# Kernel optimization log

Hardware: AMD Instinct MI355X
Metric: run time of the kernel (lower is better)

Reference implementation:

```python
import jax, jax.numpy as jnp
import numpy as np

B, S, E, H = 2, 2048, 1024, 16
D = E // H  # head dim = 64


def setup_inputs() -> dict:
    key = jax.random.key(0)
    ks = jax.random.split(key, 8)
    return {
        "query": jax.random.normal(ks[0], (B, S, E), dtype=jnp.float32),
        "key": jax.random.normal(ks[1], (B, S, E), dtype=jnp.float32),
        "value": jax.random.normal(ks[2], (B, S, E), dtype=jnp.float32),
        "qkv_weight": jax.random.normal(ks[3], (3 * E, E), dtype=jnp.float32) * 0.02,
        "qkv_bias": jax.random.normal(ks[4], (3 * E,), dtype=jnp.float32) * 0.02,
        "proj_weight": jax.random.normal(ks[5], (E, E), dtype=jnp.float32) * 0.02,
        "proj_bias": jax.random.normal(ks[6], (E,), dtype=jnp.float32) * 0.02,
        "mask": jax.random.normal(ks[7], (S, S), dtype=jnp.float32),
    }


def reference(query, key, value, qkv_weight, qkv_bias, proj_weight, proj_bias, mask):
    # Split fused QKV weight/bias into per-projection chunks ([E,E] each).
    wq, wk, wv = jnp.split(qkv_weight, 3, axis=0)
    bq, bk, bv = jnp.split(qkv_bias, 3, axis=0)

    def proj_heads(x, w, b):
        # [B,S,E] @ [E,E]^T + [E] -> [B,H,S,D]
        y = jnp.einsum("bse,fe->bsf", x, w) + b
        return y.reshape(B, S, H, D).transpose(0, 2, 1, 3)

    q = proj_heads(query, wq, bq)
    k = proj_heads(key, wk, bk)
    v = proj_heads(value, wv, bv)

    scale = 1.0 / jnp.sqrt(jnp.asarray(D, dtype=q.dtype))
    # scores: [B,H,S,S]; mask_type 0 -> additive [S,S] float mask broadcast over B,H
    scores = jnp.einsum("bhsd,bhtd->bhst", q, k) * scale + mask[None, None, :, :]
    attn = jax.nn.softmax(scores, axis=-1)
    ctx = jnp.einsum("bhst,bhtd->bhsd", attn, v)  # [B,H,S,D]
    ctx = ctx.transpose(0, 2, 1, 3).reshape(B, S, E)
    # output projection
    return jnp.einsum("bse,fe->bsf", ctx, proj_weight) + proj_bias
```

## Files before the change

### kernel.cpp

```cpp
#include <hip/hip_runtime.h>
#include <hip/hip_bf16.h>

typedef unsigned short u16;
typedef __attribute__((ext_vector_type(8))) __bf16 bf16x8;
typedef __attribute__((ext_vector_type(4))) __bf16 bf16x4;
typedef __attribute__((ext_vector_type(4))) float f32x4;

#define LOG2E 1.44269504f

#if __has_builtin(__builtin_amdgcn_exp2f)
#define EXP2F(x) __builtin_amdgcn_exp2f(x)
#else
#define EXP2F(x) __expf((x) * 0.69314718f)
#endif

#define GLL16(gptr, lptr) \
  __builtin_amdgcn_global_load_lds((__attribute__((address_space(1))) void*)(gptr), \
                                   (__attribute__((address_space(3))) void*)(lptr), 16, 0, 0)

static __device__ __forceinline__ u16 f2bf(float f) {
  union { float f; unsigned u; } v; v.f = f;
  unsigned r = (v.u + 0x7FFFu + ((v.u >> 16) & 1u)) >> 16;
  return (u16)r;
}

__global__ __launch_bounds__(256) void cvt_all(
    const float* __restrict__ q, const float* __restrict__ k, const float* __restrict__ v,
    const float* __restrict__ w1, const float* __restrict__ w2,
    u16* __restrict__ xq, u16* __restrict__ xk, u16* __restrict__ xv,
    u16* __restrict__ wq, u16* __restrict__ wp) {
  const int b = blockIdx.x;
  const float* src; u16* dst; int off;
  if (b < 4096)       { src = q;  dst = xq; off = b; }
  else if (b < 8192)  { src = k;  dst = xk; off = b - 4096; }
  else if (b < 12288) { src = v;  dst = xv; off = b - 8192; }
  else if (b < 15360) { src = w1; dst = wq; off = b - 12288; }
  else                { src = w2; dst = wp; off = b - 15360; }
  const int i = off * 256 + threadIdx.x;
  float4 vv = ((const float4*)src)[i];
  ushort4 o;
  o.x = f2bf(vv.x); o.y = f2bf(vv.y); o.z = f2bf(vv.z); o.w = f2bf(vv.w);
  ((ushort4*)dst)[i] = o;
}

__global__ __launch_bounds__(256, 2) void qkv_gemm(
    const u16* __restrict__ xq, const u16* __restrict__ xk, const u16* __restrict__ xv,
    const u16* __restrict__ wbf, const float* __restrict__ bias,
    u16* __restrict__ qout, u16* __restrict__ kout, u16* __restrict__ vtout) {
  __shared__ u16 Al[128 * 32];
  __shared__ u16 Bl[128 * 32];
  const int tid = threadIdx.x;
  const int lane = tid & 63;
  const int w = tid >> 6;
  const int wr = w >> 1, wc = w & 1;
  const int nb = blockIdx.x, mb = blockIdx.y;
  const int row0 = mb * 128;
  const int ncol0 = nb * 128;
  const int which = nb >> 3;
  const u16* A = (which == 0) ? xq : (which == 1) ? xk : xv;
  const u16* Bw = wbf + (size_t)ncol0 * 1024;

  f32x4 acc[4][4];
  f32x4 zero = {0.f, 0.f, 0.f, 0.f};
#pragma unroll
  for (int i = 0; i < 4; i++)
#pragma unroll
    for (int j = 0; j < 4; j++) acc[i][j] = zero;

  const int srow = w * 16 + (lane >> 2);
  const int scol = (lane & 3) * 8;

  for (int k0 = 0; k0 < 1024; k0 += 32) {
#pragma unroll
    for (int p = 0; p < 2; p++) {
      const u16* ga = A + (size_t)(row0 + p * 64 + srow) * 1024 + k0 + scol;
      GLL16(ga, &Al[(p * 64 + w * 16) * 32]);
      const u16* gb = Bw + (size_t)(p * 64 + srow) * 1024 + k0 + scol;
      GLL16(gb, &Bl[(p * 64 + w * 16) * 32]);
    }
    __syncthreads();
    bf16x8 af[4], bfr[4];
#pragma unroll
    for (int mi = 0; mi < 4; mi++)
      af[mi] = *(const bf16x8*)&Al[(wr * 64 + mi * 16 + (lane & 15)) * 32 + (lane >> 4) * 8];
#pragma unroll
    for (int ni = 0; ni < 4; ni++)
      bfr[ni] = *(const bf16x8*)&Bl[(wc * 64 + ni * 16 + (lane & 15)) * 32 + (lane >> 4) * 8];
#pragma unroll
    for (int mi = 0; mi < 4; mi++)
#pragma unroll
      for (int ni = 0; ni < 4; ni++)
        acc[mi][ni] = __builtin_amdgcn_mfma_f32_16x16x32_bf16(af[mi], bfr[ni], acc[mi][ni], 0, 0, 0);
    __syncthreads();
  }

#pragma unroll
  for (int mi = 0; mi < 4; mi++) {
    const int rb = row0 + wr * 64 + mi * 16 + (lane >> 4) * 4;
#pragma unroll
    for (int ni = 0; ni < 4; ni++) {
      const int c = ncol0 + wc * 64 + ni * 16 + (lane & 15);
      const float bs = bias[c];
      const float sc = (which == 0) ? (0.125f * LOG2E) : 1.0f;
      const int fm = c & 1023;
      const int h = fm >> 6, d = fm & 63;
#pragma unroll
      for (int r = 0; r < 4; r++) {
        const int rr = rb + r;
        const int b = rr >> 11, s = rr & 2047;
        const u16 val = f2bf((acc[mi][ni][r] + bs) * sc);
        if (which == 0)
          qout[(((size_t)(b * 16 + h)) * 2048 + s) * 64 + d] = val;
        else if (which == 1)
          kout[(((size_t)(b * 16 + h)) * 2048 + s) * 64 + d] = val;
        else
          vtout[(((size_t)(b * 16 + h)) * 64 + d) * 2048 + s] = val;
      }
    }
  }
}


#define STAGE_KV(KOFF, VOFF)                                        \
  *(float4*)(ldsb + (KOFF) + S0) = kr0;                             \
  *(float2*)(ldsb + (VOFF) + VS0a) = make_float2(vr0.x, vr0.y);     \
  *(float2*)(ldsb + (VOFF) + VS0b) = make_float2(vr0.z, vr0.w);

#define ATTN_TILE(PAR, MC)                                                         \
  {                                                                                \
    f32x4 s0_, s1_, s2_, s3_;                                                      \
    __builtin_amdgcn_s_setprio(1);                                                 \
    {                                                                              \
      bf16x8 a_, b_;                                                               \
      a_ = *(const bf16x8*)(ldsb + Kr0 + 0 + (PAR));                               \
      b_ = *(const bf16x8*)(ldsb + Kr1 + 0 + (PAR));                               \
      s0_ = __builtin_amdgcn_mfma_f32_16x16x32_bf16(a_, q0, MC[0], 0, 0, 0);       \
      s0_ = __builtin_amdgcn_mfma_f32_16x16x32_bf16(b_, q1, s0_, 0, 0, 0);         \
      a_ = *(const bf16x8*)(ldsb + Kr0 + 2048 + (PAR));                            \
      b_ = *(const bf16x8*)(ldsb + Kr1 + 2048 + (PAR));                            \
      s1_ = __builtin_amdgcn_mfma_f32_16x16x32_bf16(a_, q0, MC[1], 0, 0, 0);       \
      s1_ = __builtin_amdgcn_mfma_f32_16x16x32_bf16(b_, q1, s1_, 0, 0, 0);         \
      a_ = *(const bf16x8*)(ldsb + Kr0 + 4096 + (PAR));                            \
      b_ = *(const bf16x8*)(ldsb + Kr1 + 4096 + (PAR));                            \
      s2_ = __builtin_amdgcn_mfma_f32_16x16x32_bf16(a_, q0, MC[2], 0, 0, 0);       \
      s2_ = __builtin_amdgcn_mfma_f32_16x16x32_bf16(b_, q1, s2_, 0, 0, 0);         \
      a_ = *(const bf16x8*)(ldsb + Kr0 + 6144 + (PAR));                            \
      b_ = *(const bf16x8*)(ldsb + Kr1 + 6144 + (PAR));                            \
      s3_ = __builtin_amdgcn_mfma_f32_16x16x32_bf16(a_, q0, MC[3], 0, 0, 0);       \
      s3_ = __builtin_amdgcn_mfma_f32_16x16x32_bf16(b_, q1, s3_, 0, 0, 0);         \
    }                                                                              \
    __builtin_amdgcn_s_setprio(0);                                                 \
    float pm = fmaxf(fmaxf(fmaxf(fmaxf(s0_[0], s0_[1]), fmaxf(s0_[2], s0_[3])),    \
                           fmaxf(fmaxf(s1_[0], s1_[1]), fmaxf(s1_[2], s1_[3]))),   \
                     fmaxf(fmaxf(fmaxf(s2_[0], s2_[1]), fmaxf(s2_[2], s2_[3])),    \
                           fmaxf(fmaxf(s3_[0], s3_[1]), fmaxf(s3_[2], s3_[3]))));  \
                     \
    s0_[0] = EXP2F(s0_[0] - m); s0_[1] = EXP2F(s0_[1] - m);                        \
    s0_[2] = EXP2F(s0_[2] - m); s0_[3] = EXP2F(s0_[3] - m);                        \
    s1_[0] = EXP2F(s1_[0] - m); s1_[1] = EXP2F(s1_[1] - m);                        \
    s1_[2] = EXP2F(s1_[2] - m); s1_[3] = EXP2F(s1_[3] - m);                        \
    s2_[0] = EXP2F(s2_[0] - m); s2_[1] = EXP2F(s2_[1] - m);                        \
    s2_[2] = EXP2F(s2_[2] - m); s2_[3] = EXP2F(s2_[3] - m);                        \
    s3_[0] = EXP2F(s3_[0] - m); s3_[1] = EXP2F(s3_[1] - m);                        \
    s3_[2] = EXP2F(s3_[2] - m); s3_[3] = EXP2F(s3_[3] - m);                        \
    float ps = ((s0_[0] + s0_[1]) + (s0_[2] + s0_[3])) +                           \
               ((s1_[0] + s1_[1]) + (s1_[2] + s1_[3])) +                           \
               ((s2_[0] + s2_[1]) + (s2_[2] + s2_[3])) +                           \
               ((s3_[0] + s3_[1]) + (s3_[2] + s3_[3]));                            \
    pm = fmaxf(pm, __shfl_xor(pm, 16));                                            \
    pm = fmaxf(pm, __shfl_xor(pm, 32));                                            \
    if (__any(pm > m + 8.0f)) {                 \
      const float mn = fmaxf(m, pm);                                               \
      const float al = EXP2F(m - mn);                                              \
      m = mn; lsum *= al; ps *= al;                                                \
      s0_ *= al; s1_ *= al; s2_ *= al; s3_ *= al;                                  \
      ctx[0] *= al; ctx[1] *= al; ctx[2] *= al; ctx[3] *= al;                      \
    }                                                                              \
    lsum += ps;                                                                    \
           \
    bf16x8 pa0, pa1;                                                               \
    pa0[0] = (__bf16)s0_[0]; pa0[1] = (__bf16)s0_[1];                              \
    pa0[2] = (__bf16)s0_[2]; pa0[3] = (__bf16)s0_[3];                              \
    pa0[4] = (__bf16)s1_[0]; pa0[5] = (__bf16)s1_[1];                              \
    pa0[6] = (__bf16)s1_[2]; pa0[7] = (__bf16)s1_[3];                              \
    pa1[0] = (__bf16)s2_[0]; pa1[1] = (__bf16)s2_[1];                              \
    pa1[2] = (__bf16)s2_[2]; pa1[3] = (__bf16)s2_[3];                              \
    pa1[4] = (__bf16)s3_[0]; pa1[5] = (__bf16)s3_[1];                              \
    pa1[6] = (__bf16)s3_[2]; pa1[7] = (__bf16)s3_[3];                              \
    {                                                                              \
      bf16x8 v00 = *(const bf16x8*)(ldsb + Kr0 + 16384 + (PAR));                   \
      bf16x8 v01 = *(const bf16x8*)(ldsb + Kr1 + 16384 + (PAR));                   \
      bf16x8 v10 = *(const bf16x8*)(ldsb + Kr0 + 18432 + (PAR));                   \
      bf16x8 v11 = *(const bf16x8*)(ldsb + Kr1 + 18432 + (PAR));                   \
      bf16x8 v20 = *(const bf16x8*)(ldsb + Kr0 + 20480 + (PAR));                   \
      bf16x8 v21 = *(const bf16x8*)(ldsb + Kr1 + 20480 + (PAR));                   \
      bf16x8 v30 = *(const bf16x8*)(ldsb + Kr0 + 22528 + (PAR));                   \
      bf16x8 v31 = *(const bf16x8*)(ldsb + Kr1 + 22528 + (PAR));                   \
      __builtin_amdgcn_s_setprio(1);                                               \
      ctx[0] = __builtin_amdgcn_mfma_f32_16x16x32_bf16(v00, pa0, ctx[0], 0, 0, 0); \
      ctx[0] = __builtin_amdgcn_mfma_f32_16x16x32_bf16(v01, pa1, ctx[0], 0, 0, 0); \
      ctx[1] = __builtin_amdgcn_mfma_f32_16x16x32_bf16(v10, pa0, ctx[1], 0, 0, 0); \
      ctx[1] = __builtin_amdgcn_mfma_f32_16x16x32_bf16(v11, pa1, ctx[1], 0, 0, 0); \
      ctx[2] = __builtin_amdgcn_mfma_f32_16x16x32_bf16(v20, pa0, ctx[2], 0, 0, 0); \
      ctx[2] = __builtin_amdgcn_mfma_f32_16x16x32_bf16(v21, pa1, ctx[2], 0, 0, 0); \
      ctx[3] = __builtin_amdgcn_mfma_f32_16x16x32_bf16(v30, pa0, ctx[3], 0, 0, 0); \
      ctx[3] = __builtin_amdgcn_mfma_f32_16x16x32_bf16(v31, pa1, ctx[3], 0, 0, 0); \
      __builtin_amdgcn_s_setprio(0);                                               \
    }                                                                              \
  }

__global__ __launch_bounds__(512, 4) void attn_fwd(
    const u16* __restrict__ qbf, const u16* __restrict__ kbf, const u16* __restrict__ vtbf,
    const float* __restrict__ mask, u16* __restrict__ ctxout) {
  __shared__ u16 lds[16384];
  char* ldsb = (char*)lds;
  const int tid = threadIdx.x, lane = tid & 63, w = tid >> 6;
  const int qL = lane & 15, g = lane >> 4;
  const int x = (qL & 7) << 4;
  const int bh = blockIdx.x, qt = blockIdx.y;
  const int qbase = qt * 128;
  const size_t hbase = (size_t)bh * 2048 * 64;
  const int qrow = qbase + w * 16 + qL;

  const int Kr0 = qL * 128 + ((g * 16) ^ x);
  const int Kr1 = qL * 128 + ((g * 16 + 64) ^ x);
  const int srow = tid >> 3;
  const int scol = (tid & 7) * 8;
  const int S0 = srow * 128 + (((tid & 7) * 16) ^ ((srow & 7) << 4));
  const int a_ = tid & 7;
  const int vW1 = ((a_ >> 2) << 6) + (((2 * a_) & 3) << 4) + (((a_ >> 1) & 1) << 3);
  const int vW2 = ((a_ >> 2) << 6) + (((2 * a_ + 1) & 3) << 4) + (((a_ >> 1) & 1) << 3);
  const int sxr = (srow & 7) << 4;
  const int VS0a = srow * 128 + (vW1 ^ sxr);
  const int VS0b = srow * 128 + (vW2 ^ sxr);

  bf16x8 q0 = *(const bf16x8*)&qbf[hbase + (size_t)qrow * 64 + g * 8];
  bf16x8 q1 = *(const bf16x8*)&qbf[hbase + (size_t)qrow * 64 + 32 + g * 8];

  float4 kr0, vr0;
  kr0 = *(const float4*)&kbf[hbase + (size_t)srow * 64 + scol];
  vr0 = *(const float4*)&vtbf[hbase + (size_t)srow * 2048 + scol];
  STAGE_KV(0, 16384)
  kr0 = *(const float4*)&kbf[hbase + (size_t)(64 + srow) * 64 + scol];
  vr0 = *(const float4*)&vtbf[hbase + (size_t)srow * 2048 + 64 + scol];

  const u16* kp = kbf + hbase + (size_t)(128 + srow) * 64 + scol;
  const u16* vp = vtbf + hbase + (size_t)srow * 2048 + 128 + scol;
  const float* mp = mask + (size_t)qrow * 2048 + g * 4;

  f32x4 mA[4], mB[4];
#pragma unroll
  for (int tb = 0; tb < 4; tb++)
    mA[tb] = (*(const f32x4*)(mp + tb * 16)) * LOG2E;

  float m = 0.f, lsum = 0.f;
  f32x4 ctx[4];
  f32x4 zero = {0.f, 0.f, 0.f, 0.f};
#pragma unroll
  for (int db = 0; db < 4; db++) ctx[db] = zero;

  __syncthreads();

  for (int i = 0; i < 16; ++i) {
    STAGE_KV(8192, 24576)
    if (i < 15) {
      kr0 = *(const float4*)kp;
      vr0 = *(const float4*)vp;
      kp += 4096; vp += 64;
    }
#pragma unroll
    for (int tb = 0; tb < 4; tb++)
      mB[tb] = (*(const f32x4*)(mp + 64 + tb * 16)) * LOG2E;
    ATTN_TILE(0, mA)
    __syncthreads();

    if (i < 15) {
      STAGE_KV(0, 16384)
      kr0 = *(const float4*)kp;
      vr0 = *(const float4*)vp;
      kp += 4096; vp += 64;
#pragma unroll
      for (int tb = 0; tb < 4; tb++)
        mA[tb] = (*(const f32x4*)(mp + 128 + tb * 16)) * LOG2E;
    }
    ATTN_TILE(8192, mB)
    mp += 128;
    __syncthreads();
  }

  lsum += __shfl_xor(lsum, 16);
  lsum += __shfl_xor(lsum, 32);
  const float inv = 1.0f / lsum;
  const int b = bh >> 4, h = bh & 15;
  u16* orow = ctxout + (size_t)(b * 2048 + qrow) * 1024 + h * 64;
#pragma unroll
  for (int db = 0; db < 4; db++) {
    bf16x4 o;
    o[0] = (__bf16)(ctx[db][0] * inv);
    o[1] = (__bf16)(ctx[db][1] * inv);
    o[2] = (__bf16)(ctx[db][2] * inv);
    o[3] = (__bf16)(ctx[db][3] * inv);
    *(bf16x4*)&orow[db * 16 + g * 4] = o;
  }
}

__global__ __launch_bounds__(256, 2) void proj_gemm(
    const u16* __restrict__ ctx, const u16* __restrict__ wbf,
    const float* __restrict__ bias, float* __restrict__ out) {
  __shared__ u16 Al[128 * 32];
  __shared__ u16 Bl[128 * 32];
  const int tid = threadIdx.x;
  const int lane = tid & 63;
  const int w = tid >> 6;
  const int wr = w >> 1, wc = w & 1;
  const int nb = blockIdx.x, mb = blockIdx.y;
  const int row0 = mb * 128;
  const int ncol0 = nb * 128;
  const u16* Bw = wbf + (size_t)ncol0 * 1024;

  f32x4 acc[4][4];
  f32x4 zero = {0.f, 0.f, 0.f, 0.f};
#pragma unroll
  for (int i = 0; i < 4; i++)
#pragma unroll
    for (int j = 0; j < 4; j++) acc[i][j] = zero;

  const int srow = w * 16 + (lane >> 2);
  const int scol = (lane & 3) * 8;

  for (int k0 = 0; k0 < 1024; k0 += 32) {
#pragma unroll
    for (int p = 0; p < 2; p++) {
      const u16* ga = ctx + (size_t)(row0 + p * 64 + srow) * 1024 + k0 + scol;
      GLL16(ga, &Al[(p * 64 + w * 16) * 32]);
      const u16* gb = Bw + (size_t)(p * 64 + srow) * 1024 + k0 + scol;
      GLL16(gb, &Bl[(p * 64 + w * 16) * 32]);
    }
    __syncthreads();
    bf16x8 af[4], bfr[4];
#pragma unroll
    for (int mi = 0; mi < 4; mi++)
      af[mi] = *(const bf16x8*)&Al[(wr * 64 + mi * 16 + (lane & 15)) * 32 + (lane >> 4) * 8];
#pragma unroll
    for (int ni = 0; ni < 4; ni++)
      bfr[ni] = *(const bf16x8*)&Bl[(wc * 64 + ni * 16 + (lane & 15)) * 32 + (lane >> 4) * 8];
#pragma unroll
    for (int mi = 0; mi < 4; mi++)
#pragma unroll
      for (int ni = 0; ni < 4; ni++)
        acc[mi][ni] = __builtin_amdgcn_mfma_f32_16x16x32_bf16(af[mi], bfr[ni], acc[mi][ni], 0, 0, 0);
    __syncthreads();
  }

#pragma unroll
  for (int mi = 0; mi < 4; mi++) {
    const int rb = row0 + wr * 64 + mi * 16 + (lane >> 4) * 4;
#pragma unroll
    for (int ni = 0; ni < 4; ni++) {
      const int c = ncol0 + wc * 64 + ni * 16 + (lane & 15);
      const float bs = bias[c];
#pragma unroll
      for (int r = 0; r < 4; r++)
        out[(size_t)(rb + r) * 1024 + c] = acc[mi][ni][r] + bs;
    }
  }
}

extern "C" void kernel_launch(void* const* d_in, const int* in_sizes, int n_in,
                              void* d_out, int out_size, void* d_ws, size_t ws_size,
                              hipStream_t stream) {
  const float* query = (const float*)d_in[0];
  const float* key   = (const float*)d_in[1];
  const float* value = (const float*)d_in[2];
  const float* qkvw  = (const float*)d_in[3];
  const float* qkvb  = (const float*)d_in[4];
  const float* projw = (const float*)d_in[5];
  const float* projb = (const float*)d_in[6];
  const float* mask  = (const float*)d_in[7];

  char* ws = (char*)d_ws;
  u16* xq    = (u16*)(ws + 0);
  u16* xk    = (u16*)(ws + 8388608);
  u16* xv    = (u16*)(ws + 16777216);
  u16* wqkv  = (u16*)(ws + 25165824);
  u16* wproj = (u16*)(ws + 31457280);
  u16* qb    = (u16*)(ws + 33554432);
  u16* kb    = (u16*)(ws + 41943040);
  u16* vt    = (u16*)(ws + 50331648);
  u16* cx    = xq;

  cvt_all<<<16384, 256, 0, stream>>>(query, key, value, qkvw, projw, xq, xk, xv, wqkv, wproj);
  qkv_gemm<<<dim3(24, 32), 256, 0, stream>>>(xq, xk, xv, wqkv, qkvb, qb, kb, vt);
  attn_fwd<<<dim3(32, 16), 512, 0, stream>>>(qb, kb, vt, mask, cx);
  proj_gemm<<<dim3(8, 32), 256, 0, stream>>>(cx, wproj, projb, (float*)d_out);
}
```

Baseline: 160.9 us.

## Process 128-key blocks per softmax step with double-buffered K/V in LDS

```diff
diff --git a/kernel.cpp b/kernel.cpp
--- a/kernel.cpp
+++ b/kernel.cpp
@@ -121,98 +121,56 @@
 }
 
 
-#define STAGE_KV(KOFF, VOFF)                                        \
-  *(float4*)(ldsb + (KOFF) + S0) = kr0;                             \
-  *(float2*)(ldsb + (VOFF) + VS0a) = make_float2(vr0.x, vr0.y);     \
-  *(float2*)(ldsb + (VOFF) + VS0b) = make_float2(vr0.z, vr0.w);
-
-#define ATTN_TILE(PAR, MC)                                                         \
+#define QK4(SS0, SS1, SS2, SS3, KOFF, MC)                                          \
   {                                                                                \
-    f32x4 s0_, s1_, s2_, s3_;                                                      \
-    __builtin_amdgcn_s_setprio(1);                                                 \
-    {                                                                              \
-      bf16x8 a_, b_;                                                               \
-      a_ = *(const bf16x8*)(ldsb + Kr0 + 0 + (PAR));                               \
-      b_ = *(const bf16x8*)(ldsb + Kr1 + 0 + (PAR));                               \
-      s0_ = __builtin_amdgcn_mfma_f32_16x16x32_bf16(a_, q0, MC[0], 0, 0, 0);       \
-      s0_ = __builtin_amdgcn_mfma_f32_16x16x32_bf16(b_, q1, s0_, 0, 0, 0);         \
-      a_ = *(const bf16x8*)(ldsb + Kr0 + 2048 + (PAR));                            \
-      b_ = *(const bf16x8*)(ldsb + Kr1 + 2048 + (PAR));                            \
-      s1_ = __builtin_amdgcn_mfma_f32_16x16x32_bf16(a_, q0, MC[1], 0, 0, 0);       \
-      s1_ = __builtin_amdgcn_mfma_f32_16x16x32_bf16(b_, q1, s1_, 0, 0, 0);         \
-      a_ = *(const bf16x8*)(ldsb + Kr0 + 4096 + (PAR));                            \
-      b_ = *(const bf16x8*)(ldsb + Kr1 + 4096 + (PAR));                            \
-      s2_ = __builtin_amdgcn_mfma_f32_16x16x32_bf16(a_, q0, MC[2], 0, 0, 0);       \
-      s2_ = __builtin_amdgcn_mfma_f32_16x16x32_bf16(b_, q1, s2_, 0, 0, 0);         \
-      a_ = *(const bf16x8*)(ldsb + Kr0 + 6144 + (PAR));                            \
-      b_ = *(const bf16x8*)(ldsb + Kr1 + 6144 + (PAR));                            \
-      s3_ = __builtin_amdgcn_mfma_f32_16x16x32_bf16(a_, q0, MC[3], 0, 0, 0);       \
-      s3_ = __builtin_amdgcn_mfma_f32_16x16x32_bf16(b_, q1, s3_, 0, 0, 0);         \
-    }                                                                              \
-    __builtin_amdgcn_s_setprio(0);                                                 \
-    float pm = fmaxf(fmaxf(fmaxf(fmaxf(s0_[0], s0_[1]), fmaxf(s0_[2], s0_[3])),    \
-                           fmaxf(fmaxf(s1_[0], s1_[1]), fmaxf(s1_[2], s1_[3]))),   \
-                     fmaxf(fmaxf(fmaxf(s2_[0], s2_[1]), fmaxf(s2_[2], s2_[3])),    \
-                           fmaxf(fmaxf(s3_[0], s3_[1]), fmaxf(s3_[2], s3_[3]))));  \
-                     \
-    s0_[0] = EXP2F(s0_[0] - m); s0_[1] = EXP2F(s0_[1] - m);                        \
-    s0_[2] = EXP2F(s0_[2] - m); s0_[3] = EXP2F(s0_[3] - m);                        \
-    s1_[0] = EXP2F(s1_[0] - m); s1_[1] = EXP2F(s1_[1] - m);                        \
-    s1_[2] = EXP2F(s1_[2] - m); s1_[3] = EXP2F(s1_[3] - m);                        \
-    s2_[0] = EXP2F(s2_[0] - m); s2_[1] = EXP2F(s2_[1] - m);                        \
-    s2_[2] = EXP2F(s2_[2] - m); s2_[3] = EXP2F(s2_[3] - m);                        \
-    s3_[0] = EXP2F(s3_[0] - m); s3_[1] = EXP2F(s3_[1] - m);                        \
-    s3_[2] = EXP2F(s3_[2] - m); s3_[3] = EXP2F(s3_[3] - m);                        \
-    float ps = ((s0_[0] + s0_[1]) + (s0_[2] + s0_[3])) +                           \
-               ((s1_[0] + s1_[1]) + (s1_[2] + s1_[3])) +                           \
-               ((s2_[0] + s2_[1]) + (s2_[2] + s2_[3])) +                           \
-               ((s3_[0] + s3_[1]) + (s3_[2] + s3_[3]));                            \
-    pm = fmaxf(pm, __shfl_xor(pm, 16));                                            \
-    pm = fmaxf(pm, __shfl_xor(pm, 32));                                            \
-    if (__any(pm > m + 8.0f)) {                 \
-      const float mn = fmaxf(m, pm);                                               \
-      const float al = EXP2F(m - mn);                                              \
-      m = mn; lsum *= al; ps *= al;                                                \
-      s0_ *= al; s1_ *= al; s2_ *= al; s3_ *= al;                                  \
-      ctx[0] *= al; ctx[1] *= al; ctx[2] *= al; ctx[3] *= al;                      \
-    }                                                                              \
-    lsum += ps;                                                                    \
-           \
-    bf16x8 pa0, pa1;                                                               \
-    pa0[0] = (__bf16)s0_[0]; pa0[1] = (__bf16)s0_[1];                              \
-    pa0[2] = (__bf16)s0_[2]; pa0[3] = (__bf16)s0_[3];                              \
-    pa0[4] = (__bf16)s1_[0]; pa0[5] = (__bf16)s1_[1];                              \
-    pa0[6] = (__bf16)s1_[2]; pa0[7] = (__bf16)s1_[3];                              \
-    pa1[0] = (__bf16)s2_[0]; pa1[1] = (__bf16)s2_[1];                              \
-    pa1[2] = (__bf16)s2_[2]; pa1[3] = (__bf16)s2_[3];                              \
-    pa1[4] = (__bf16)s3_[0]; pa1[5] = (__bf16)s3_[1];                              \
-    pa1[6] = (__bf16)s3_[2]; pa1[7] = (__bf16)s3_[3];                              \
-    {                                                                              \
-      bf16x8 v00 = *(const bf16x8*)(ldsb + Kr0 + 16384 + (PAR));                   \
-      bf16x8 v01 = *(const bf16x8*)(ldsb + Kr1 + 16384 + (PAR));                   \
-      bf16x8 v10 = *(const bf16x8*)(ldsb + Kr0 + 18432 + (PAR));                   \
-      bf16x8 v11 = *(const bf16x8*)(ldsb + Kr1 + 18432 + (PAR));                   \
-      bf16x8 v20 = *(const bf16x8*)(ldsb + Kr0 + 20480 + (PAR));                   \
-      bf16x8 v21 = *(const bf16x8*)(ldsb + Kr1 + 20480 + (PAR));                   \
-      bf16x8 v30 = *(const bf16x8*)(ldsb + Kr0 + 22528 + (PAR));                   \
-      bf16x8 v31 = *(const bf16x8*)(ldsb + Kr1 + 22528 + (PAR));                   \
-      __builtin_amdgcn_s_setprio(1);                                               \
-      ctx[0] = __builtin_amdgcn_mfma_f32_16x16x32_bf16(v00, pa0, ctx[0], 0, 0, 0); \
-      ctx[0] = __builtin_amdgcn_mfma_f32_16x16x32_bf16(v01, pa1, ctx[0], 0, 0, 0); \
-      ctx[1] = __builtin_amdgcn_mfma_f32_16x16x32_bf16(v10, pa0, ctx[1], 0, 0, 0); \
-      ctx[1] = __builtin_amdgcn_mfma_f32_16x16x32_bf16(v11, pa1, ctx[1], 0, 0, 0); \
-      ctx[2] = __builtin_amdgcn_mfma_f32_16x16x32_bf16(v20, pa0, ctx[2], 0, 0, 0); \
-      ctx[2] = __builtin_amdgcn_mfma_f32_16x16x32_bf16(v21, pa1, ctx[2], 0, 0, 0); \
-      ctx[3] = __builtin_amdgcn_mfma_f32_16x16x32_bf16(v30, pa0, ctx[3], 0, 0, 0); \
-      ctx[3] = __builtin_amdgcn_mfma_f32_16x16x32_bf16(v31, pa1, ctx[3], 0, 0, 0); \
-      __builtin_amdgcn_s_setprio(0);                                               \
-    }                                                                              \
-  }
+    bf16x8 a_, b_;                                                                 \
+    a_ = *(const bf16x8*)(ldsb + Kr0 + 0 + (KOFF));                                \
+    b_ = *(const bf16x8*)(ldsb + Kr1 + 0 + (KOFF));                                \
+    SS0 = __builtin_amdgcn_mfma_f32_16x16x32_bf16(a_, q0, MC[0], 0, 0, 0);         \
+    SS0 = __builtin_amdgcn_mfma_f32_16x16x32_bf16(b_, q1, SS0, 0, 0, 0);           \
+    a_ = *(const bf16x8*)(ldsb + Kr0 + 2048 + (KOFF));                             \
+    b_ = *(const bf16x8*)(ldsb + Kr1 + 2048 + (KOFF));                             \
+    SS1 = __builtin_amdgcn_mfma_f32_16x16x32_bf16(a_, q0, MC[1], 0, 0, 0);         \
+    SS1 = __builtin_amdgcn_mfma_f32_16x16x32_bf16(b_, q1, SS1, 0, 0, 0);           \
+    a_ = *(const bf16x8*)(ldsb + Kr0 + 4096 + (KOFF));                             \
+    b_ = *(const bf16x8*)(ldsb + Kr1 + 4096 + (KOFF));                             \
+    SS2 = __builtin_amdgcn_mfma_f32_16x16x32_bf16(a_, q0, MC[2], 0, 0, 0);         \
+    SS2 = __builtin_amdgcn_mfma_f32_16x16x32_bf16(b_, q1, SS2, 0, 0, 0);           \
+    a_ = *(const bf16x8*)(ldsb + Kr0 + 6144 + (KOFF));                             \
+    b_ = *(const bf16x8*)(ldsb + Kr1 + 6144 + (KOFF));                             \
+    SS3 = __builtin_amdgcn_mfma_f32_16x16x32_bf16(a_, q0, MC[3], 0, 0, 0);         \
+    SS3 = __builtin_amdgcn_mfma_f32_16x16x32_bf16(b_, q1, SS3, 0, 0, 0);           \
+  }
+
+#define PV8(PA0, PA1, VOFF)                                                        \
+  {                                                                                \
+    bf16x8 v0_, v1_;                                                               \
+    v0_ = *(const bf16x8*)(ldsb + Kr0 + 0 + (VOFF));                               \
+    v1_ = *(const bf16x8*)(ldsb + Kr1 + 0 + (VOFF));                               \
+    ctx[0] = __builtin_amdgcn_mfma_f32_16x16x32_bf16(v0_, PA0, ctx[0], 0, 0, 0);   \
+    ctx[0] = __builtin_amdgcn_mfma_f32_16x16x32_bf16(v1_, PA1, ctx[0], 0, 0, 0);   \
+    v0_ = *(const bf16x8*)(ldsb + Kr0 + 2048 + (VOFF));                            \
+    v1_ = *(const bf16x8*)(ldsb + Kr1 + 2048 + (VOFF));                            \
+    ctx[1] = __builtin_amdgcn_mfma_f32_16x16x32_bf16(v0_, PA0, ctx[1], 0, 0, 0);   \
+    ctx[1] = __builtin_amdgcn_mfma_f32_16x16x32_bf16(v1_, PA1, ctx[1], 0, 0, 0);   \
+    v0_ = *(const bf16x8*)(ldsb + Kr0 + 4096 + (VOFF));                            \
+    v1_ = *(const bf16x8*)(ldsb + Kr1 + 4096 + (VOFF));                            \
+    ctx[2] = __builtin_amdgcn_mfma_f32_16x16x32_bf16(v0_, PA0, ctx[2], 0, 0, 0);   \
+    ctx[2] = __builtin_amdgcn_mfma_f32_16x16x32_bf16(v1_, PA1, ctx[2], 0, 0, 0);   \
+    v0_ = *(const bf16x8*)(ldsb + Kr0 + 6144 + (VOFF));                            \
+    v1_ = *(const bf16x8*)(ldsb + Kr1 + 6144 + (VOFF));                            \
+    ctx[3] = __builtin_amdgcn_mfma_f32_16x16x32_bf16(v0_, PA0, ctx[3], 0, 0, 0);   \
+    ctx[3] = __builtin_amdgcn_mfma_f32_16x16x32_bf16(v1_, PA1, ctx[3], 0, 0, 0);   \
+  }
+
+#define EXPV(SS)                                                                   \
+  SS[0] = EXP2F(SS[0] - m); SS[1] = EXP2F(SS[1] - m);                              \
+  SS[2] = EXP2F(SS[2] - m); SS[3] = EXP2F(SS[3] - m);
 
 __global__ __launch_bounds__(512, 4) void attn_fwd(
     const u16* __restrict__ qbf, const u16* __restrict__ kbf, const u16* __restrict__ vtbf,
     const float* __restrict__ mask, u16* __restrict__ ctxout) {
-  __shared__ u16 lds[16384];
+  __shared__ u16 lds[32768];
   char* ldsb = (char*)lds;
   const int tid = threadIdx.x, lane = tid & 63, w = tid >> 6;
   const int qL = lane & 15, g = lane >> 4;
@@ -237,21 +195,32 @@
   bf16x8 q0 = *(const bf16x8*)&qbf[hbase + (size_t)qrow * 64 + g * 8];
   bf16x8 q1 = *(const bf16x8*)&qbf[hbase + (size_t)qrow * 64 + 32 + g * 8];
 
-  float4 kr0, vr0;
+  float4 kr0, kr1, vr0, vr1;
   kr0 = *(const float4*)&kbf[hbase + (size_t)srow * 64 + scol];
+  kr1 = *(const float4*)&kbf[hbase + (size_t)(64 + srow) * 64 + scol];
   vr0 = *(const float4*)&vtbf[hbase + (size_t)srow * 2048 + scol];
-  STAGE_KV(0, 16384)
-  kr0 = *(const float4*)&kbf[hbase + (size_t)(64 + srow) * 64 + scol];
-  vr0 = *(const float4*)&vtbf[hbase + (size_t)srow * 2048 + 64 + scol];
-
-  const u16* kp = kbf + hbase + (size_t)(128 + srow) * 64 + scol;
-  const u16* vp = vtbf + hbase + (size_t)srow * 2048 + 128 + scol;
+  vr1 = *(const float4*)&vtbf[hbase + (size_t)srow * 2048 + 64 + scol];
+  *(float4*)(ldsb + S0) = kr0;
+  *(float4*)(ldsb + 8192 + S0) = kr1;
+  *(float2*)(ldsb + 32768 + VS0a) = make_float2(vr0.x, vr0.y);
+  *(float2*)(ldsb + 32768 + VS0b) = make_float2(vr0.z, vr0.w);
+  *(float2*)(ldsb + 40960 + VS0a) = make_float2(vr1.x, vr1.y);
+  *(float2*)(ldsb + 40960 + VS0b) = make_float2(vr1.z, vr1.w);
+  kr0 = *(const float4*)&kbf[hbase + (size_t)(128 + srow) * 64 + scol];
+  kr1 = *(const float4*)&kbf[hbase + (size_t)(192 + srow) * 64 + scol];
+  vr0 = *(const float4*)&vtbf[hbase + (size_t)srow * 2048 + 128 + scol];
+  vr1 = *(const float4*)&vtbf[hbase + (size_t)srow * 2048 + 192 + scol];
+
+  const u16* kp = kbf + hbase + (size_t)(256 + srow) * 64 + scol;
+  const u16* vp = vtbf + hbase + (size_t)srow * 2048 + 256 + scol;
   const float* mp = mask + (size_t)qrow * 2048 + g * 4;
 
   f32x4 mA[4], mB[4];
 #pragma unroll
-  for (int tb = 0; tb < 4; tb++)
+  for (int tb = 0; tb < 4; tb++) {
     mA[tb] = (*(const f32x4*)(mp + tb * 16)) * LOG2E;
+    mB[tb] = (*(const f32x4*)(mp + 64 + tb * 16)) * LOG2E;
+  }
 
   float m = 0.f, lsum = 0.f;
   f32x4 ctx[4];
@@ -262,29 +231,93 @@
   __syncthreads();
 
   for (int i = 0; i < 16; ++i) {
-    STAGE_KV(8192, 24576)
+    const int cb = (i & 1) << 14;
+    const int sb = 16384 - cb;
+    f32x4 sA0, sA1, sA2, sA3, sB0, sB1, sB2, sB3;
+
+    __builtin_amdgcn_s_setprio(1);
+    QK4(sA0, sA1, sA2, sA3, cb, mA)
+    QK4(sB0, sB1, sB2, sB3, cb + 8192, mB)
+    __builtin_amdgcn_s_setprio(0);
+
     if (i < 15) {
+      *(float4*)(ldsb + sb + S0) = kr0;
+      *(float4*)(ldsb + sb + 8192 + S0) = kr1;
+      *(float2*)(ldsb + 32768 + sb + VS0a) = make_float2(vr0.x, vr0.y);
+      *(float2*)(ldsb + 32768 + sb + VS0b) = make_float2(vr0.z, vr0.w);
+      *(float2*)(ldsb + 40960 + sb + VS0a) = make_float2(vr1.x, vr1.y);
+      *(float2*)(ldsb + 40960 + sb + VS0b) = make_float2(vr1.z, vr1.w);
+    }
+    if (i < 14) {
       kr0 = *(const float4*)kp;
+      kr1 = *(const float4*)(kp + 4096);
       vr0 = *(const float4*)vp;
-      kp += 4096; vp += 64;
-    }
-#pragma unroll
-    for (int tb = 0; tb < 4; tb++)
-      mB[tb] = (*(const f32x4*)(mp + 64 + tb * 16)) * LOG2E;
-    ATTN_TILE(0, mA)
-    __syncthreads();
-
+      vr1 = *(const float4*)(vp + 64);
+      kp += 8192; vp += 128;
+    }
     if (i < 15) {
-      STAGE_KV(0, 16384)
-      kr0 = *(const float4*)kp;
-      vr0 = *(const float4*)vp;
-      kp += 4096; vp += 64;
-#pragma unroll
-      for (int tb = 0; tb < 4; tb++)
+#pragma unroll
+      for (int tb = 0; tb < 4; tb++) {
         mA[tb] = (*(const f32x4*)(mp + 128 + tb * 16)) * LOG2E;
-    }
-    ATTN_TILE(8192, mB)
+        mB[tb] = (*(const f32x4*)(mp + 192 + tb * 16)) * LOG2E;
+      }
+    }
     mp += 128;
+
+    float pm = fmaxf(
+        fmaxf(fmaxf(fmaxf(fmaxf(sA0[0], sA0[1]), fmaxf(sA0[2], sA0[3])),
+                    fmaxf(fmaxf(sA1[0], sA1[1]), fmaxf(sA1[2], sA1[3]))),
+              fmaxf(fmaxf(fmaxf(sA2[0], sA2[1]), fmaxf(sA2[2], sA2[3])),
+                    fmaxf(fmaxf(sA3[0], sA3[1]), fmaxf(sA3[2], sA3[3])))),
+        fmaxf(fmaxf(fmaxf(fmaxf(sB0[0], sB0[1]), fmaxf(sB0[2], sB0[3])),
+                    fmaxf(fmaxf(sB1[0], sB1[1]), fmaxf(sB1[2], sB1[3]))),
+              fmaxf(fmaxf(fmaxf(sB2[0], sB2[1]), fmaxf(sB2[2], sB2[3])),
+                    fmaxf(fmaxf(sB3[0], sB3[1]), fmaxf(sB3[2], sB3[3])))));
+    EXPV(sA0) EXPV(sA1) EXPV(sA2) EXPV(sA3)
+    EXPV(sB0) EXPV(sB1) EXPV(sB2) EXPV(sB3)
+    float ps = (((sA0[0] + sA0[1]) + (sA0[2] + sA0[3])) +
+                ((sA1[0] + sA1[1]) + (sA1[2] + sA1[3]))) +
+               (((sA2[0] + sA2[1]) + (sA2[2] + sA2[3])) +
+                ((sA3[0] + sA3[1]) + (sA3[2] + sA3[3]))) +
+               (((sB0[0] + sB0[1]) + (sB0[2] + sB0[3])) +
+                ((sB1[0] + sB1[1]) + (sB1[2] + sB1[3]))) +
+               (((sB2[0] + sB2[1]) + (sB2[2] + sB2[3])) +
+                ((sB3[0] + sB3[1]) + (sB3[2] + sB3[3])));
+    pm = fmaxf(pm, __shfl_xor(pm, 16));
+    pm = fmaxf(pm, __shfl_xor(pm, 32));
+    if (__any(pm > m + 8.0f)) {
+      const float mn = fmaxf(m, pm);
+      const float al = EXP2F(m - mn);
+      m = mn; lsum *= al; ps *= al;
+      sA0 *= al; sA1 *= al; sA2 *= al; sA3 *= al;
+      sB0 *= al; sB1 *= al; sB2 *= al; sB3 *= al;
+      ctx[0] *= al; ctx[1] *= al; ctx[2] *= al; ctx[3] *= al;
+    }
+    lsum += ps;
+
+    bf16x8 paA0, paA1, paB0, paB1;
+    paA0[0] = (__bf16)sA0[0]; paA0[1] = (__bf16)sA0[1];
+    paA0[2] = (__bf16)sA0[2]; paA0[3] = (__bf16)sA0[3];
+    paA0[4] = (__bf16)sA1[0]; paA0[5] = (__bf16)sA1[1];
+    paA0[6] = (__bf16)sA1[2]; paA0[7] = (__bf16)sA1[3];
+    paA1[0] = (__bf16)sA2[0]; paA1[1] = (__bf16)sA2[1];
+    paA1[2] = (__bf16)sA2[2]; paA1[3] = (__bf16)sA2[3];
+    paA1[4] = (__bf16)sA3[0]; paA1[5] = (__bf16)sA3[1];
+    paA1[6] = (__bf16)sA3[2]; paA1[7] = (__bf16)sA3[3];
+    paB0[0] = (__bf16)sB0[0]; paB0[1] = (__bf16)sB0[1];
+    paB0[2] = (__bf16)sB0[2]; paB0[3] = (__bf16)sB0[3];
+    paB0[4] = (__bf16)sB1[0]; paB0[5] = (__bf16)sB1[1];
+    paB0[6] = (__bf16)sB1[2]; paB0[7] = (__bf16)sB1[3];
+    paB1[0] = (__bf16)sB2[0]; paB1[1] = (__bf16)sB2[1];
+    paB1[2] = (__bf16)sB2[2]; paB1[3] = (__bf16)sB2[3];
+    paB1[4] = (__bf16)sB3[0]; paB1[5] = (__bf16)sB3[1];
+    paB1[6] = (__bf16)sB3[2]; paB1[7] = (__bf16)sB3[3];
+
+    __builtin_amdgcn_s_setprio(1);
+    PV8(paA0, paA1, 32768 + cb)
+    PV8(paB0, paB1, 40960 + cb)
+    __builtin_amdgcn_s_setprio(0);
+
     __syncthreads();
   }
 
```

Result: slower. 175.1 us (+8.9%).

## Switch attention kernel to 32x32x16 MFMA with 4 waves of 32 queries each

Applied to the files above, without the earlier changes.

```diff
diff --git a/kernel.cpp b/kernel.cpp
--- a/kernel.cpp
+++ b/kernel.cpp
@@ -5,6 +5,7 @@
 typedef __attribute__((ext_vector_type(8))) __bf16 bf16x8;
 typedef __attribute__((ext_vector_type(4))) __bf16 bf16x4;
 typedef __attribute__((ext_vector_type(4))) float f32x4;
+typedef __attribute__((ext_vector_type(16))) float f32x16;
 
 #define LOG2E 1.44269504f
 
@@ -121,186 +122,198 @@
 }
 
 
-#define STAGE_KV(KOFF, VOFF)                                        \
-  *(float4*)(ldsb + (KOFF) + S0) = kr0;                             \
-  *(float2*)(ldsb + (VOFF) + VS0a) = make_float2(vr0.x, vr0.y);     \
-  *(float2*)(ldsb + (VOFF) + VS0b) = make_float2(vr0.z, vr0.w);
-
-#define ATTN_TILE(PAR, MC)                                                         \
+#define MFMA32(A, B, C) __builtin_amdgcn_mfma_f32_32x32x16_bf16(A, B, C, 0, 0, 0)
+
+#define TILE_BODY(KOFF, MA, MB)                                                    \
   {                                                                                \
-    f32x4 s0_, s1_, s2_, s3_;                                                      \
+    f32x16 sA, sB;                                                                 \
     __builtin_amdgcn_s_setprio(1);                                                 \
     {                                                                              \
-      bf16x8 a_, b_;                                                               \
-      a_ = *(const bf16x8*)(ldsb + Kr0 + 0 + (PAR));                               \
-      b_ = *(const bf16x8*)(ldsb + Kr1 + 0 + (PAR));                               \
-      s0_ = __builtin_amdgcn_mfma_f32_16x16x32_bf16(a_, q0, MC[0], 0, 0, 0);       \
-      s0_ = __builtin_amdgcn_mfma_f32_16x16x32_bf16(b_, q1, s0_, 0, 0, 0);         \
-      a_ = *(const bf16x8*)(ldsb + Kr0 + 2048 + (PAR));                            \
-      b_ = *(const bf16x8*)(ldsb + Kr1 + 2048 + (PAR));                            \
-      s1_ = __builtin_amdgcn_mfma_f32_16x16x32_bf16(a_, q0, MC[1], 0, 0, 0);       \
-      s1_ = __builtin_amdgcn_mfma_f32_16x16x32_bf16(b_, q1, s1_, 0, 0, 0);         \
-      a_ = *(const bf16x8*)(ldsb + Kr0 + 4096 + (PAR));                            \
-      b_ = *(const bf16x8*)(ldsb + Kr1 + 4096 + (PAR));                            \
-      s2_ = __builtin_amdgcn_mfma_f32_16x16x32_bf16(a_, q0, MC[2], 0, 0, 0);       \
-      s2_ = __builtin_amdgcn_mfma_f32_16x16x32_bf16(b_, q1, s2_, 0, 0, 0);         \
-      a_ = *(const bf16x8*)(ldsb + Kr0 + 6144 + (PAR));                            \
-      b_ = *(const bf16x8*)(ldsb + Kr1 + 6144 + (PAR));                            \
-      s3_ = __builtin_amdgcn_mfma_f32_16x16x32_bf16(a_, q0, MC[3], 0, 0, 0);       \
-      s3_ = __builtin_amdgcn_mfma_f32_16x16x32_bf16(b_, q1, s3_, 0, 0, 0);         \
+      const char* kb0 = ldsb + (KOFF) + Kb;                                        \
+      sA = MFMA32(*(const bf16x8*)(kb0 + o0), qf0, MA);                            \
+      sB = MFMA32(*(const bf16x8*)(kb0 + 4096 + o0), qf0, MB);                     \
+      sA = MFMA32(*(const bf16x8*)(kb0 + o1), qf1, sA);                            \
+      sB = MFMA32(*(const bf16x8*)(kb0 + 4096 + o1), qf1, sB);                     \
+      sA = MFMA32(*(const bf16x8*)(kb0 + o2), qf2, sA);                            \
+      sB = MFMA32(*(const bf16x8*)(kb0 + 4096 + o2), qf2, sB);                     \
+      sA = MFMA32(*(const bf16x8*)(kb0 + o3), qf3, sA);                            \
+      sB = MFMA32(*(const bf16x8*)(kb0 + 4096 + o3), qf3, sB);                     \
     }                                                                              \
     __builtin_amdgcn_s_setprio(0);                                                 \
-    float pm = fmaxf(fmaxf(fmaxf(fmaxf(s0_[0], s0_[1]), fmaxf(s0_[2], s0_[3])),    \
-                           fmaxf(fmaxf(s1_[0], s1_[1]), fmaxf(s1_[2], s1_[3]))),   \
-                     fmaxf(fmaxf(fmaxf(s2_[0], s2_[1]), fmaxf(s2_[2], s2_[3])),    \
-                           fmaxf(fmaxf(s3_[0], s3_[1]), fmaxf(s3_[2], s3_[3]))));  \
+    float pm = fmaxf(                                                              \
+        fmaxf(fmaxf(fmaxf(fmaxf(sA[0], sA[1]), fmaxf(sA[2], sA[3])),               \
+                    fmaxf(fmaxf(sA[4], sA[5]), fmaxf(sA[6], sA[7]))),              \
+              fmaxf(fmaxf(fmaxf(sA[8], sA[9]), fmaxf(sA[10], sA[11])),             \
+                    fmaxf(fmaxf(sA[12], sA[13]), fmaxf(sA[14], sA[15])))),         \
+        fmaxf(fmaxf(fmaxf(fmaxf(sB[0], sB[1]), fmaxf(sB[2], sB[3])),               \
+                    fmaxf(fmaxf(sB[4], sB[5]), fmaxf(sB[6], sB[7]))),              \
+              fmaxf(fmaxf(fmaxf(sB[8], sB[9]), fmaxf(sB[10], sB[11])),             \
+                    fmaxf(fmaxf(sB[12], sB[13]), fmaxf(sB[14], sB[15])))));        \
                      \
-    s0_[0] = EXP2F(s0_[0] - m); s0_[1] = EXP2F(s0_[1] - m);                        \
-    s0_[2] = EXP2F(s0_[2] - m); s0_[3] = EXP2F(s0_[3] - m);                        \
-    s1_[0] = EXP2F(s1_[0] - m); s1_[1] = EXP2F(s1_[1] - m);                        \
-    s1_[2] = EXP2F(s1_[2] - m); s1_[3] = EXP2F(s1_[3] - m);                        \
-    s2_[0] = EXP2F(s2_[0] - m); s2_[1] = EXP2F(s2_[1] - m);                        \
-    s2_[2] = EXP2F(s2_[2] - m); s2_[3] = EXP2F(s2_[3] - m);                        \
-    s3_[0] = EXP2F(s3_[0] - m); s3_[1] = EXP2F(s3_[1] - m);                        \
-    s3_[2] = EXP2F(s3_[2] - m); s3_[3] = EXP2F(s3_[3] - m);                        \
-    float ps = ((s0_[0] + s0_[1]) + (s0_[2] + s0_[3])) +                           \
-               ((s1_[0] + s1_[1]) + (s1_[2] + s1_[3])) +                           \
-               ((s2_[0] + s2_[1]) + (s2_[2] + s2_[3])) +                           \
-               ((s3_[0] + s3_[1]) + (s3_[2] + s3_[3]));                            \
-    pm = fmaxf(pm, __shfl_xor(pm, 16));                                            \
+    _Pragma("unroll")                                                              \
+    for (int e_ = 0; e_ < 16; e_++) { sA[e_] = EXP2F(sA[e_] - m); }                \
+    _Pragma("unroll")                                                              \
+    for (int e_ = 0; e_ < 16; e_++) { sB[e_] = EXP2F(sB[e_] - m); }                \
+    float ps = (((sA[0] + sA[1]) + (sA[2] + sA[3])) +                              \
+                ((sA[4] + sA[5]) + (sA[6] + sA[7]))) +                             \
+               (((sA[8] + sA[9]) + (sA[10] + sA[11])) +                            \
+                ((sA[12] + sA[13]) + (sA[14] + sA[15]))) +                         \
+               (((sB[0] + sB[1]) + (sB[2] + sB[3])) +                              \
+                ((sB[4] + sB[5]) + (sB[6] + sB[7]))) +                             \
+               (((sB[8] + sB[9]) + (sB[10] + sB[11])) +                            \
+                ((sB[12] + sB[13]) + (sB[14] + sB[15])));                          \
     pm = fmaxf(pm, __shfl_xor(pm, 32));                                            \
     if (__any(pm > m + 8.0f)) {                 \
       const float mn = fmaxf(m, pm);                                               \
       const float al = EXP2F(m - mn);                                              \
       m = mn; lsum *= al; ps *= al;                                                \
-      s0_ *= al; s1_ *= al; s2_ *= al; s3_ *= al;                                  \
-      ctx[0] *= al; ctx[1] *= al; ctx[2] *= al; ctx[3] *= al;                      \
+      sA *= al; sB *= al; ctx0 *= al; ctx1 *= al;                                  \
     }                                                                              \
     lsum += ps;                                                                    \
-           \
-    bf16x8 pa0, pa1;                                                               \
-    pa0[0] = (__bf16)s0_[0]; pa0[1] = (__bf16)s0_[1];                              \
-    pa0[2] = (__bf16)s0_[2]; pa0[3] = (__bf16)s0_[3];                              \
-    pa0[4] = (__bf16)s1_[0]; pa0[5] = (__bf16)s1_[1];                              \
-    pa0[6] = (__bf16)s1_[2]; pa0[7] = (__bf16)s1_[3];                              \
-    pa1[0] = (__bf16)s2_[0]; pa1[1] = (__bf16)s2_[1];                              \
-    pa1[2] = (__bf16)s2_[2]; pa1[3] = (__bf16)s2_[3];                              \
-    pa1[4] = (__bf16)s3_[0]; pa1[5] = (__bf16)s3_[1];                              \
-    pa1[6] = (__bf16)s3_[2]; pa1[7] = (__bf16)s3_[3];                              \
+    bf16x8 pa0, pa1, pa2, pa3;                                                     \
+    _Pragma("unroll")                                                              \
+    for (int e_ = 0; e_ < 8; e_++) {                                               \
+      pa0[e_] = (__bf16)sA[e_]; pa1[e_] = (__bf16)sA[8 + e_];                      \
+      pa2[e_] = (__bf16)sB[e_]; pa3[e_] = (__bf16)sB[8 + e_];                      \
+    }                                                                              \
     {                                                                              \
-      bf16x8 v00 = *(const bf16x8*)(ldsb + Kr0 + 16384 + (PAR));                   \
-      bf16x8 v01 = *(const bf16x8*)(ldsb + Kr1 + 16384 + (PAR));                   \
-      bf16x8 v10 = *(const bf16x8*)(ldsb + Kr0 + 18432 + (PAR));                   \
-      bf16x8 v11 = *(const bf16x8*)(ldsb + Kr1 + 18432 + (PAR));                   \
-      bf16x8 v20 = *(const bf16x8*)(ldsb + Kr0 + 20480 + (PAR));                   \
-      bf16x8 v21 = *(const bf16x8*)(ldsb + Kr1 + 20480 + (PAR));                   \
-      bf16x8 v30 = *(const bf16x8*)(ldsb + Kr0 + 22528 + (PAR));                   \
-      bf16x8 v31 = *(const bf16x8*)(ldsb + Kr1 + 22528 + (PAR));                   \
+      const char* vb0 = ldsb + 16384 + (KOFF) + Vb;                                \
       __builtin_amdgcn_s_setprio(1);                                               \
-      ctx[0] = __builtin_amdgcn_mfma_f32_16x16x32_bf16(v00, pa0, ctx[0], 0, 0, 0); \
-      ctx[0] = __builtin_amdgcn_mfma_f32_16x16x32_bf16(v01, pa1, ctx[0], 0, 0, 0); \
-      ctx[1] = __builtin_amdgcn_mfma_f32_16x16x32_bf16(v10, pa0, ctx[1], 0, 0, 0); \
-      ctx[1] = __builtin_amdgcn_mfma_f32_16x16x32_bf16(v11, pa1, ctx[1], 0, 0, 0); \
-      ctx[2] = __builtin_amdgcn_mfma_f32_16x16x32_bf16(v20, pa0, ctx[2], 0, 0, 0); \
-      ctx[2] = __builtin_amdgcn_mfma_f32_16x16x32_bf16(v21, pa1, ctx[2], 0, 0, 0); \
-      ctx[3] = __builtin_amdgcn_mfma_f32_16x16x32_bf16(v30, pa0, ctx[3], 0, 0, 0); \
-      ctx[3] = __builtin_amdgcn_mfma_f32_16x16x32_bf16(v31, pa1, ctx[3], 0, 0, 0); \
+      ctx0 = MFMA32(*(const bf16x8*)(vb0 + 0), pa0, ctx0);                         \
+      ctx1 = MFMA32(*(const bf16x8*)(vb0 + 1024), pa0, ctx1);                      \
+      ctx0 = MFMA32(*(const bf16x8*)(vb0 + 2048), pa1, ctx0);                      \
+      ctx1 = MFMA32(*(const bf16x8*)(vb0 + 3072), pa1, ctx1);                      \
+      ctx0 = MFMA32(*(const bf16x8*)(vb0 + 4096), pa2, ctx0);                      \
+      ctx1 = MFMA32(*(const bf16x8*)(vb0 + 5120), pa2, ctx1);                      \
+      ctx0 = MFMA32(*(const bf16x8*)(vb0 + 6144), pa3, ctx0);                      \
+      ctx1 = MFMA32(*(const bf16x8*)(vb0 + 7168), pa3, ctx1);                      \
       __builtin_amdgcn_s_setprio(0);                                               \
     }                                                                              \
   }
 
-__global__ __launch_bounds__(512, 4) void attn_fwd(
+__global__ __launch_bounds__(256, 2) void attn_fwd(
     const u16* __restrict__ qbf, const u16* __restrict__ kbf, const u16* __restrict__ vtbf,
     const float* __restrict__ mask, u16* __restrict__ ctxout) {
   __shared__ u16 lds[16384];
   char* ldsb = (char*)lds;
   const int tid = threadIdx.x, lane = tid & 63, w = tid >> 6;
-  const int qL = lane & 15, g = lane >> 4;
-  const int x = (qL & 7) << 4;
+  const int q32 = lane & 31, hi = lane >> 5;
   const int bh = blockIdx.x, qt = blockIdx.y;
   const int qbase = qt * 128;
   const size_t hbase = (size_t)bh * 2048 * 64;
-  const int qrow = qbase + w * 16 + qL;
-
-  const int Kr0 = qL * 128 + ((g * 16) ^ x);
-  const int Kr1 = qL * 128 + ((g * 16 + 64) ^ x);
-  const int srow = tid >> 3;
-  const int scol = (tid & 7) * 8;
-  const int S0 = srow * 128 + (((tid & 7) * 16) ^ ((srow & 7) << 4));
-  const int a_ = tid & 7;
-  const int vW1 = ((a_ >> 2) << 6) + (((2 * a_) & 3) << 4) + (((a_ >> 1) & 1) << 3);
-  const int vW2 = ((a_ >> 2) << 6) + (((2 * a_ + 1) & 3) << 4) + (((a_ >> 1) & 1) << 3);
-  const int sxr = (srow & 7) << 4;
-  const int VS0a = srow * 128 + (vW1 ^ sxr);
-  const int VS0b = srow * 128 + (vW2 ^ sxr);
-
-  bf16x8 q0 = *(const bf16x8*)&qbf[hbase + (size_t)qrow * 64 + g * 8];
-  bf16x8 q1 = *(const bf16x8*)&qbf[hbase + (size_t)qrow * 64 + 32 + g * 8];
-
-  float4 kr0, vr0;
-  kr0 = *(const float4*)&kbf[hbase + (size_t)srow * 64 + scol];
-  vr0 = *(const float4*)&vtbf[hbase + (size_t)srow * 2048 + scol];
-  STAGE_KV(0, 16384)
-  kr0 = *(const float4*)&kbf[hbase + (size_t)(64 + srow) * 64 + scol];
-  vr0 = *(const float4*)&vtbf[hbase + (size_t)srow * 2048 + 64 + scol];
-
-  const u16* kp = kbf + hbase + (size_t)(128 + srow) * 64 + scol;
-  const u16* vp = vtbf + hbase + (size_t)srow * 2048 + 128 + scol;
-  const float* mp = mask + (size_t)qrow * 2048 + g * 4;
-
-  f32x4 mA[4], mB[4];
-#pragma unroll
-  for (int tb = 0; tb < 4; tb++)
-    mA[tb] = (*(const f32x4*)(mp + tb * 16)) * LOG2E;
+  const int qglob = qbase + w * 32 + q32;
+
+  const int x = (q32 & 7) << 4;
+  const int Kb = q32 * 128;
+  const int o0 = (0 + hi * 16) ^ x;
+  const int o1 = (32 + hi * 16) ^ x;
+  const int o2 = (64 + hi * 16) ^ x;
+  const int o3 = (96 + hi * 16) ^ x;
+  const int Vb = hi * 512 + q32 * 16;
+  const int srow = tid >> 3, Ac = tid & 7;
+  const int S0 = srow * 128 + ((Ac * 16) ^ ((srow & 7) << 4));
+  const int S1 = S0 + 4096;
+  const int jv = Ac >> 1, epos = (Ac & 1) * 8;
+  const int VW0 = jv * 2048 + srow * 16 + epos;
+  const int VW1 = jv * 2048 + 1024 + srow * 16 + epos;
+
+  const u16* qrow = qbf + hbase + (size_t)qglob * 64 + hi * 8;
+  bf16x8 qf0 = *(const bf16x8*)(qrow + 0);
+  bf16x8 qf1 = *(const bf16x8*)(qrow + 16);
+  bf16x8 qf2 = *(const bf16x8*)(qrow + 32);
+  bf16x8 qf3 = *(const bf16x8*)(qrow + 48);
+
+  float4 kr0, kr1, vr0, vr1;
+  kr0 = *(const float4*)&kbf[hbase + (size_t)srow * 64 + Ac * 8];
+  kr1 = *(const float4*)&kbf[hbase + (size_t)(32 + srow) * 64 + Ac * 8];
+  vr0 = *(const float4*)&vtbf[hbase + (size_t)srow * 2048 + Ac * 8];
+  vr1 = *(const float4*)&vtbf[hbase + (size_t)(32 + srow) * 2048 + Ac * 8];
+  *(float4*)(ldsb + S0) = kr0;
+  *(float4*)(ldsb + S1) = kr1;
+  *(float2*)(ldsb + 16384 + VW0) = make_float2(vr0.x, vr0.y);
+  *(float2*)(ldsb + 16384 + VW0 + 512) = make_float2(vr0.z, vr0.w);
+  *(float2*)(ldsb + 16384 + VW1) = make_float2(vr1.x, vr1.y);
+  *(float2*)(ldsb + 16384 + VW1 + 512) = make_float2(vr1.z, vr1.w);
+  kr0 = *(const float4*)&kbf[hbase + (size_t)(64 + srow) * 64 + Ac * 8];
+  kr1 = *(const float4*)&kbf[hbase + (size_t)(96 + srow) * 64 + Ac * 8];
+  vr0 = *(const float4*)&vtbf[hbase + (size_t)srow * 2048 + 64 + Ac * 8];
+  vr1 = *(const float4*)&vtbf[hbase + (size_t)(32 + srow) * 2048 + 64 + Ac * 8];
+
+  const u16* kp = kbf + hbase + (size_t)(128 + srow) * 64 + Ac * 8;
+  const u16* vp = vtbf + hbase + (size_t)srow * 2048 + 128 + Ac * 8;
+  const float* mpp = mask + (size_t)qglob * 2048 + hi * 4;
+
+  f32x16 mcA, mcB, mdA, mdB;
+#pragma unroll
+  for (int jq = 0; jq < 4; jq++) {
+    ((f32x4*)&mcA)[jq] = (*(const f32x4*)(mpp + jq * 8)) * LOG2E;
+    ((f32x4*)&mcB)[jq] = (*(const f32x4*)(mpp + 32 + jq * 8)) * LOG2E;
+  }
 
   float m = 0.f, lsum = 0.f;
-  f32x4 ctx[4];
-  f32x4 zero = {0.f, 0.f, 0.f, 0.f};
-#pragma unroll
-  for (int db = 0; db < 4; db++) ctx[db] = zero;
+  f32x16 ctx0 = (f32x16)(0.f), ctx1 = (f32x16)(0.f);
 
   __syncthreads();
 
   for (int i = 0; i < 16; ++i) {
-    STAGE_KV(8192, 24576)
+    *(float4*)(ldsb + 8192 + S0) = kr0;
+    *(float4*)(ldsb + 8192 + S1) = kr1;
+    *(float2*)(ldsb + 24576 + VW0) = make_float2(vr0.x, vr0.y);
+    *(float2*)(ldsb + 24576 + VW0 + 512) = make_float2(vr0.z, vr0.w);
+    *(float2*)(ldsb + 24576 + VW1) = make_float2(vr1.x, vr1.y);
+    *(float2*)(ldsb + 24576 + VW1 + 512) = make_float2(vr1.z, vr1.w);
     if (i < 15) {
       kr0 = *(const float4*)kp;
+      kr1 = *(const float4*)(kp + 2048);
       vr0 = *(const float4*)vp;
+      vr1 = *(const float4*)(vp + 65536);
       kp += 4096; vp += 64;
     }
 #pragma unroll
-    for (int tb = 0; tb < 4; tb++)
-      mB[tb] = (*(const f32x4*)(mp + 64 + tb * 16)) * LOG2E;
-    ATTN_TILE(0, mA)
+    for (int jq = 0; jq < 4; jq++) {
+      ((f32x4*)&mdA)[jq] = (*(const f32x4*)(mpp + 64 + jq * 8)) * LOG2E;
+      ((f32x4*)&mdB)[jq] = (*(const f32x4*)(mpp + 96 + jq * 8)) * LOG2E;
+    }
+    TILE_BODY(0, mcA, mcB)
     __syncthreads();
 
     if (i < 15) {
-      STAGE_KV(0, 16384)
+      *(float4*)(ldsb + S0) = kr0;
+      *(float4*)(ldsb + S1) = kr1;
+      *(float2*)(ldsb + 16384 + VW0) = make_float2(vr0.x, vr0.y);
+      *(float2*)(ldsb + 16384 + VW0 + 512) = make_float2(vr0.z, vr0.w);
+      *(float2*)(ldsb + 16384 + VW1) = make_float2(vr1.x, vr1.y);
+      *(float2*)(ldsb + 16384 + VW1 + 512) = make_float2(vr1.z, vr1.w);
       kr0 = *(const float4*)kp;
+      kr1 = *(const float4*)(kp + 2048);
       vr0 = *(const float4*)vp;
+      vr1 = *(const float4*)(vp + 65536);
       kp += 4096; vp += 64;
 #pragma unroll
-      for (int tb = 0; tb < 4; tb++)
-        mA[tb] = (*(const f32x4*)(mp + 128 + tb * 16)) * LOG2E;
-    }
-    ATTN_TILE(8192, mB)
-    mp += 128;
-    __syncthreads();
-  }
-
-  lsum += __shfl_xor(lsum, 16);
+      for (int jq = 0; jq < 4; jq++) {
+        ((f32x4*)&mcA)[jq] = (*(const f32x4*)(mpp + 128 + jq * 8)) * LOG2E;
+        ((f32x4*)&mcB)[jq] = (*(const f32x4*)(mpp + 160 + jq * 8)) * LOG2E;
+      }
+    }
+    TILE_BODY(8192, mdA, mdB)
+    mpp += 128;
+    __syncthreads();
+  }
+
   lsum += __shfl_xor(lsum, 32);
   const float inv = 1.0f / lsum;
   const int b = bh >> 4, h = bh & 15;
-  u16* orow = ctxout + (size_t)(b * 2048 + qrow) * 1024 + h * 64;
-#pragma unroll
-  for (int db = 0; db < 4; db++) {
-    bf16x4 o;
-    o[0] = (__bf16)(ctx[db][0] * inv);
-    o[1] = (__bf16)(ctx[db][1] * inv);
-    o[2] = (__bf16)(ctx[db][2] * inv);
-    o[3] = (__bf16)(ctx[db][3] * inv);
-    *(bf16x4*)&orow[db * 16 + g * 4] = o;
+  u16* orow = ctxout + (size_t)(b * 2048 + qglob) * 1024 + h * 64;
+#pragma unroll
+  for (int jq = 0; jq < 4; jq++) {
+    bf16x4 o0, o1;
+#pragma unroll
+    for (int rr = 0; rr < 4; rr++) {
+      o0[rr] = (__bf16)(ctx0[4 * jq + rr] * inv);
+      o1[rr] = (__bf16)(ctx1[4 * jq + rr] * inv);
+    }
+    *(bf16x4*)&orow[jq * 8 + hi * 4] = o0;
+    *(bf16x4*)&orow[32 + jq * 8 + hi * 4] = o1;
   }
 }
 
@@ -391,6 +404,6 @@
 
   cvt_all<<<16384, 256, 0, stream>>>(query, key, value, qkvw, projw, xq, xk, xv, wqkv, wproj);
   qkv_gemm<<<dim3(24, 32), 256, 0, stream>>>(xq, xk, xv, wqkv, qkvb, qb, kb, vt);
-  attn_fwd<<<dim3(32, 16), 512, 0, stream>>>(qb, kb, vt, mask, cx);
+  attn_fwd<<<dim3(32, 16), 256, 0, stream>>>(qb, kb, vt, mask, cx);
   proj_gemm<<<dim3(8, 32), 256, 0, stream>>>(cx, wproj, projb, (float*)d_out);
 }
```

Measured after the change: 169.2 us. 1.05x slower.
